# Kernel tuning notes

Measured on AMD Instinct MI355X. Metric: run time of the kernel, lower is better.

The kernel has to match this reference:

```python
import jax, jax.numpy as jnp
import numpy as np
from jax.ops import segment_sum

N = 100000   # nodes
E = 1600000  # edges
F = 128      # node feature dim
H = 128      # hidden dim
FE = 16      # edge feature dim
G = 256      # num graphs
EPS = 1e-5   # batch-norm eps


def setup_inputs() -> dict:
    key = jax.random.key(0)
    ks = jax.random.split(key, 16)
    s = 0.05
    return {
        "x": jax.random.normal(ks[0], (N, F), jnp.float32),
        "edge_index": jax.random.randint(ks[1], (2, E), 0, N, dtype=jnp.int32),
        "edge_attr": jax.random.normal(ks[2], (E, FE), jnp.float32),
        "batch_idx": jnp.sort(jax.random.randint(ks[3], (N,), 0, G, dtype=jnp.int32)),
        # GCN layer 1
        "W_g1": jax.random.normal(ks[4], (F, H), jnp.float32) * s,
        "b_g1": jnp.zeros((H,), jnp.float32),
        "gamma1": jnp.ones((H,), jnp.float32),
        "beta1": jnp.zeros((H,), jnp.float32),
        # GCN layer 2
        "W_g2": jax.random.normal(ks[5], (H, H), jnp.float32) * s,
        "b_g2": jnp.zeros((H,), jnp.float32),
        "gamma2": jnp.ones((H,), jnp.float32),
        "beta2": jnp.zeros((H,), jnp.float32),
        # edge encoder MLP
        "W_e1": jax.random.normal(ks[6], (FE, H), jnp.float32) * s,
        "b_e1": jnp.zeros((H,), jnp.float32),
        "W_e2": jax.random.normal(ks[7], (H, H), jnp.float32) * s,
        "b_e2": jnp.zeros((H,), jnp.float32),
    }


def _gcn_bn_relu(x, src, dst, W, b, gamma, beta):
    """GCNConv (sym-normalized, self-loops) + BatchNorm1d (batch stats) + ReLU."""
    h = x @ W                                             # [N, H]
    ones = jnp.ones((E,), h.dtype)
    deg = segment_sum(ones, dst, num_segments=N) + 1.0    # self-loop degree
    dinv = jax.lax.rsqrt(deg)                             # [N]
    norm = dinv[src] * dinv[dst]                          # [E]
    agg = segment_sum(h[src] * norm[:, None], dst, num_segments=N)
    out = agg + h * (dinv * dinv)[:, None] + b            # self-loop + bias
    mu = out.mean(axis=0)
    var = out.var(axis=0)
    out = (out - mu) * jax.lax.rsqrt(var + EPS) * gamma + beta
    return jax.nn.relu(out)


def reference(x, edge_index, edge_attr, batch_idx, W_g1, b_g1, gamma1, beta1,
              W_g2, b_g2, gamma2, beta2, W_e1, b_e1, W_e2, b_e2):
    src, dst = edge_index[0], edge_index[1]
    h = _gcn_bn_relu(x, src, dst, W_g1, b_g1, gamma1, beta1)
    h = _gcn_bn_relu(h, src, dst, W_g2, b_g2, gamma2, beta2)

    # global mean pool over nodes per graph
    node_cnt = segment_sum(jnp.ones((N,), h.dtype), batch_idx, num_segments=G)
    graph_repr = segment_sum(h, batch_idx, num_segments=G) / jnp.maximum(node_cnt, 1.0)[:, None]

    # edge encoder MLP + per-graph edge mean (vectorized version of the loop)
    e = jax.nn.relu(edge_attr @ W_e1 + b_e1) @ W_e2 + b_e2   # [E, H]
    edge_batch = batch_idx[src]                              # [E]
    edge_cnt = segment_sum(jnp.ones((E,), e.dtype), edge_batch, num_segments=G)
    edge_sum = segment_sum(e, edge_batch, num_segments=G)
    edge_repr = jnp.where(edge_cnt[:, None] > 0, edge_sum / jnp.maximum(edge_cnt, 1.0)[:, None], 0.0)

    return graph_repr + edge_repr  # [G, H]
```

## Files before the change

kernel.cpp:

```cpp
#include <hip/hip_runtime.h>
#include <cstdint>

__device__ inline unsigned int bfpack2(float a, float b) {
  unsigned int ua = __float_as_uint(a), ub = __float_as_uint(b);
  ua += 0x7FFFu + ((ua >> 16) & 1u);
  ub += 0x7FFFu + ((ub >> 16) & 1u);
  return (ua >> 16) | (ub & 0xFFFF0000u);
}
__device__ inline float bflo(unsigned int u) { return __uint_as_float(u << 16); }
__device__ inline float bfhi(unsigned int u) { return __uint_as_float(u & 0xFFFF0000u); }

__global__ __launch_bounds__(256) void pre_kernel(const int* __restrict__ src,
                                                  const int* __restrict__ dst,
                                                  int* __restrict__ deg,
                                                  int* __restrict__ deg2, int nE) {
  int e = blockIdx.x * 256 + threadIdx.x;
  if (e < nE) {
    atomicAdd(&deg[dst[e]], 1);
    atomicAdd(&deg2[src[e]], 1);
  }
}

__global__ __launch_bounds__(256) void scanA_kernel(const int* __restrict__ deg,
                                                    const int* __restrict__ deg2,
                                                    int* __restrict__ rp,
                                                    int* __restrict__ rp2,
                                                    int* __restrict__ part,
                                                    int* __restrict__ part2,
                                                    int n, int nb) {
  __shared__ int sh[256];
  int b = blockIdx.x, t = threadIdx.x;
  const int* d = (b < nb) ? deg : deg2;
  int* r = (b < nb) ? rp : rp2;
  int* p = (b < nb) ? part : part2;
  int pad = (b < nb) ? 1 : 0;
  int bb = (b < nb) ? b : b - nb;
  int base = bb * 1024 + t * 4;
  int v0 = (base + 0 < n) ? d[base + 0] : 0;
  int v1 = (base + 1 < n) ? d[base + 1] : 0;
  int v2 = (base + 2 < n) ? d[base + 2] : 0;
  int v3 = (base + 3 < n) ? d[base + 3] : 0;
  if (pad) {
    v0 = (v0 + 7) & ~7; v1 = (v1 + 7) & ~7;
    v2 = (v2 + 7) & ~7; v3 = (v3 + 7) & ~7;
  }
  int ts = v0 + v1 + v2 + v3;
  sh[t] = ts;
  __syncthreads();
  for (int off = 1; off < 256; off <<= 1) {
    int x = (t >= off) ? sh[t - off] : 0;
    __syncthreads();
    sh[t] += x;
    __syncthreads();
  }
  int excl = sh[t] - ts;
  if (t == 255) p[bb] = sh[255];
  if (base + 0 < n) r[base + 0] = excl;
  if (base + 1 < n) r[base + 1] = excl + v0;
  if (base + 2 < n) r[base + 2] = excl + v0 + v1;
  if (base + 3 < n) r[base + 3] = excl + v0 + v1 + v2;
}

__global__ void scanB_kernel(int* part, int* part2, int* rp, int* rp2, int nb, int n) {
  if (threadIdx.x == 0) {
    int* p = (blockIdx.x == 0) ? part : part2;
    int* r = (blockIdx.x == 0) ? rp : rp2;
    int run = 0;
    for (int i = 0; i < nb; ++i) { int v = p[i]; p[i] = run; run += v; }
    r[n] = run;
  }
}

__global__ __launch_bounds__(256) void scanC_kernel(int* __restrict__ rp,
                                                    int* __restrict__ rp2,
                                                    const int* __restrict__ part,
                                                    const int* __restrict__ part2,
                                                    int* __restrict__ cursor,
                                                    int* __restrict__ cursor2,
                                                    const int* __restrict__ deg,
                                                    float* __restrict__ dinv, int n) {
  int i = blockIdx.x * 256 + threadIdx.x;
  if (i < n) {
    int v = rp[i] + part[i >> 10];
    rp[i] = v;
    cursor[i] = v;
    dinv[i] = rsqrtf((float)deg[i] + 1.0f);
  } else if (i < 2 * n) {
    int j = i - n;
    int v = rp2[j] + part2[j >> 10];
    rp2[j] = v;
    cursor2[j] = v;
  }
}

__global__ __launch_bounds__(256) void placepad_kernel(const int* __restrict__ src,
                                                       const int* __restrict__ dst,
                                                       const int* __restrict__ batch,
                                                       const float* __restrict__ dinv,
                                                       int* __restrict__ cursor,
                                                       int* __restrict__ cursor2,
                                                       int2* __restrict__ swv,
                                                       unsigned int* __restrict__ epk,
                                                       const int* __restrict__ rp,
                                                       const int* __restrict__ deg,
                                                       int nE, int nN) {
  int t = blockIdx.x * 256 + threadIdx.x;
  if (t < nE) {
    int s = src[t];
    int d = dst[t];
    int p1 = atomicAdd(&cursor[d], 1);
    int2 sw; sw.x = s; sw.y = __float_as_int(dinv[s] * dinv[d]);
    swv[p1] = sw;
    int g = batch[s];
    int p2 = atomicAdd(&cursor2[s], 1);
    epk[p2] = ((unsigned int)g << 21) | (unsigned int)t;
  } else if (t < nE + nN) {
    int i = t - nE;
    int b = rp[i] + deg[i], e = rp[i + 1];
    int2 z; z.x = i; z.y = 0;
    for (int k = b; k < e; ++k) swv[k] = z;
  }
}

template <bool FUSED>
__global__ __launch_bounds__(256) void gemm128_kernel(const float* __restrict__ A,
                                                      const float* __restrict__ W,
                                                      const float* __restrict__ scale,
                                                      const float* __restrict__ shift,
                                                      unsigned int* __restrict__ hpk2,
                                                      int nrows) {
  extern __shared__ float lds[];
  float* Ws = lds;
  float* xs = lds + 128 * 128;
  const int t = threadIdx.x;
  for (int i = t; i < (128 * 128) / 4; i += 256)
    reinterpret_cast<float4*>(Ws)[i] = reinterpret_cast<const float4*>(W)[i];
  const int wave = t >> 6, lane = t & 63;
  const size_t sbase = (size_t)(lane >> 3) * (size_t)nrows * 8 + (lane & 7);
  for (int rb = blockIdx.x * 16; rb < nrows; rb += gridDim.x * 16) {
    int nr = min(16, nrows - rb);
    __syncthreads();
    for (int i = t; i < nr * 32; i += 256) {
      float4 v = reinterpret_cast<const float4*>(A + (size_t)rb * 128)[i];
      if (FUSED) {
        float4 sc4 = reinterpret_cast<const float4*>(scale)[i & 31];
        float4 sh4 = reinterpret_cast<const float4*>(shift)[i & 31];
        v.x = fmaxf(fmaf(v.x, sc4.x, sh4.x), 0.f);
        v.y = fmaxf(fmaf(v.y, sc4.y, sh4.y), 0.f);
        v.z = fmaxf(fmaf(v.z, sc4.z, sh4.z), 0.f);
        v.w = fmaxf(fmaf(v.w, sc4.w, sh4.w), 0.f);
      }
      reinterpret_cast<float4*>(xs)[i] = v;
    }
    __syncthreads();
    float acc[4][2] = {{0.f, 0.f}, {0.f, 0.f}, {0.f, 0.f}, {0.f, 0.f}};
    const float* xw = xs + wave * 4 * 128;
#pragma unroll 4
    for (int k = 0; k < 128; ++k) {
      float w0 = Ws[k * 128 + lane];
      float w1 = Ws[k * 128 + 64 + lane];
#pragma unroll
      for (int r = 0; r < 4; ++r) {
        float a = xw[r * 128 + k];
        acc[r][0] = fmaf(a, w0, acc[r][0]);
        acc[r][1] = fmaf(a, w1, acc[r][1]);
      }
    }
#pragma unroll
    for (int r = 0; r < 4; ++r) {
      int row = rb + wave * 4 + r;
      if (row < nrows)
        hpk2[sbase + (size_t)row * 8] = bfpack2(acc[r][0], acc[r][1]);
    }
  }
}

__global__ __launch_bounds__(256) void spmm8_kernel(const unsigned int* __restrict__ hpk2,
                                                    const float* __restrict__ dinv,
                                                    const int* __restrict__ rp,
                                                    const int2* __restrict__ swv,
                                                    const float* __restrict__ bias,
                                                    float* __restrict__ outp,
                                                    float* __restrict__ bnsum,
                                                    float* __restrict__ bnsq, int nN) {
  const int lane = threadIdx.x & 63;
  const int ch = lane & 7;
  const int es = lane >> 3;
  const int slice = blockIdx.x & 7;
  const unsigned int* hs = hpk2 + (size_t)slice * (size_t)nN * 8;
  const int cb = slice * 8;
  const int wib = (int)(blockIdx.x >> 3) * 4 + (int)(threadIdx.x >> 6);
  const int nws = (int)(gridDim.x >> 3) * 4;
  const unsigned long long* swq = reinterpret_cast<const unsigned long long*>(swv);
  float b0 = bias[cb + ch], b1 = bias[64 + cb + ch];
  float s0 = 0.f, s1 = 0.f, q0 = 0.f, q1 = 0.f;
  const int half = (nN + 1) >> 1;

#define SPMM_CHUNK(J, ACC0, ACC1)                                         \
  {                                                                       \
    unsigned long long v_ = __builtin_nontemporal_load(swq + (J) + es);   \
    unsigned int pp_ = hs[(size_t)(unsigned int)v_ * 8 + ch];             \
    float ww_ = __uint_as_float((unsigned int)(v_ >> 32));                \
    ACC0 = fmaf(ww_, bflo(pp_), ACC0);                                    \
    ACC1 = fmaf(ww_, bfhi(pp_), ACC1);                                    \
  }

  for (int p = wib; p < half; p += nws) {
    const int n0 = p;
    const int n1 = p + half;
    const bool has1 = n1 < nN;
    int j0 = rp[n0];
    const int end0 = rp[n0 + 1];
    int j1 = 0, end1 = 0;
    if (has1) { j1 = rp[n1]; end1 = rp[n1 + 1]; }
    float a00 = 0.f, a01 = 0.f, b00 = 0.f, b01 = 0.f;
    float a10 = 0.f, a11 = 0.f, b10 = 0.f, b11 = 0.f;
    while (j0 + 8 < end0 && j1 + 8 < end1) {
      SPMM_CHUNK(j0, a00, a01);
      SPMM_CHUNK(j0 + 8, b00, b01);
      SPMM_CHUNK(j1, a10, a11);
      SPMM_CHUNK(j1 + 8, b10, b11);
      j0 += 16; j1 += 16;
    }
    while (j0 + 8 < end0) {
      SPMM_CHUNK(j0, a00, a01);
      SPMM_CHUNK(j0 + 8, b00, b01);
      j0 += 16;
    }
    if (j0 < end0) SPMM_CHUNK(j0, a00, a01);
    while (j1 + 8 < end1) {
      SPMM_CHUNK(j1, a10, a11);
      SPMM_CHUNK(j1 + 8, b10, b11);
      j1 += 16;
    }
    if (j1 < end1) SPMM_CHUNK(j1, a10, a11);

    a00 += b00; a01 += b01;
    a10 += b10; a11 += b11;
    a00 += __shfl_xor(a00, 8);  a01 += __shfl_xor(a01, 8);
    a10 += __shfl_xor(a10, 8);  a11 += __shfl_xor(a11, 8);
    a00 += __shfl_xor(a00, 16); a01 += __shfl_xor(a01, 16);
    a10 += __shfl_xor(a10, 16); a11 += __shfl_xor(a11, 16);
    a00 += __shfl_xor(a00, 32); a01 += __shfl_xor(a01, 32);
    a10 += __shfl_xor(a10, 32); a11 += __shfl_xor(a11, 32);
    if (es == 0) {
      {
        float dn = dinv[n0];
        float sw = dn * dn;
        unsigned int pn = hs[(size_t)n0 * 8 + ch];
        float o0 = fmaf(bflo(pn), sw, a00) + b0;
        float o1 = fmaf(bfhi(pn), sw, a01) + b1;
        __builtin_nontemporal_store(o0, &outp[(size_t)n0 * 128 + cb + ch]);
        __builtin_nontemporal_store(o1, &outp[(size_t)n0 * 128 + 64 + cb + ch]);
        s0 += o0; s1 += o1;
        q0 = fmaf(o0, o0, q0); q1 = fmaf(o1, o1, q1);
      }
      if (has1) {
        float dn = dinv[n1];
        float sw = dn * dn;
        unsigned int pn = hs[(size_t)n1 * 8 + ch];
        float o0 = fmaf(bflo(pn), sw, a10) + b0;
        float o1 = fmaf(bfhi(pn), sw, a11) + b1;
        __builtin_nontemporal_store(o0, &outp[(size_t)n1 * 128 + cb + ch]);
        __builtin_nontemporal_store(o1, &outp[(size_t)n1 * 128 + 64 + cb + ch]);
        s0 += o0; s1 += o1;
        q0 = fmaf(o0, o0, q0); q1 = fmaf(o1, o1, q1);
      }
    }
  }
#undef SPMM_CHUNK
  if (es == 0) {
    atomicAdd(&bnsum[cb + ch], s0);
    atomicAdd(&bnsum[64 + cb + ch], s1);
    atomicAdd(&bnsq[cb + ch], q0);
    atomicAdd(&bnsq[64 + cb + ch], q1);
  }
}

__global__ void bnfin_kernel(const float* __restrict__ sum, const float* __restrict__ sq,
                             const float* __restrict__ gamma, const float* __restrict__ beta,
                             float* __restrict__ scale, float* __restrict__ shift,
                             float invN) {
  int c = threadIdx.x;
  float mu = sum[c] * invN;
  float var = sq[c] * invN - mu * mu;
  float sc = gamma[c] * rsqrtf(var + 1e-5f);
  scale[c] = sc;
  shift[c] = beta[c] - mu * sc;
}

__global__ __launch_bounds__(256) void pool_kernel(const float* __restrict__ h,
                                                   const int* __restrict__ batch,
                                                   const float* __restrict__ scale,
                                                   const float* __restrict__ shift,
                                                   float* __restrict__ gsum,
                                                   float* __restrict__ gcnt,
                                                   int nN, int chunk) {
  const int lane = threadIdx.x & 63;
  const int wid = (blockIdx.x * blockDim.x + threadIdx.x) >> 6;
  int beg = wid * chunk;
  if (beg >= nN) return;
  int end = min(nN, beg + chunk);
  const int c2 = 2 * lane;
  float2 sc2 = *reinterpret_cast<const float2*>(scale + c2);
  float2 sh2 = *reinterpret_cast<const float2*>(shift + c2);
  int cur = -1;
  float a0 = 0.f, a1 = 0.f, cnt = 0.f;
  for (int n = beg; n < end; ++n) {
    int g = batch[n];
    if (g != cur) {
      if (cur >= 0) {
        atomicAdd(&gsum[cur * 128 + c2], a0);
        atomicAdd(&gsum[cur * 128 + c2 + 1], a1);
        if (lane == 0) atomicAdd(&gcnt[cur], cnt);
      }
      cur = g; a0 = 0.f; a1 = 0.f; cnt = 0.f;
    }
    float2 v = *reinterpret_cast<const float2*>(h + (size_t)n * 128 + c2);
    a0 += fmaxf(fmaf(v.x, sc2.x, sh2.x), 0.f);
    a1 += fmaxf(fmaf(v.y, sc2.y, sh2.y), 0.f);
    cnt += 1.f;
  }
  if (cur >= 0) {
    atomicAdd(&gsum[cur * 128 + c2], a0);
    atomicAdd(&gsum[cur * 128 + c2 + 1], a1);
    if (lane == 0) atomicAdd(&gcnt[cur], cnt);
  }
}

#define MLP16(R0, R1, R2, R3, U0, U1)                          \
  do {                                                         \
    U0 = b0; U1 = b1;                                          \
    U0 = fmaf(R0.x, w0[0], U0);  U1 = fmaf(R0.x, w1[0], U1);   \
    U0 = fmaf(R0.y, w0[1], U0);  U1 = fmaf(R0.y, w1[1], U1);   \
    U0 = fmaf(R0.z, w0[2], U0);  U1 = fmaf(R0.z, w1[2], U1);   \
    U0 = fmaf(R0.w, w0[3], U0);  U1 = fmaf(R0.w, w1[3], U1);   \
    U0 = fmaf(R1.x, w0[4], U0);  U1 = fmaf(R1.x, w1[4], U1);   \
    U0 = fmaf(R1.y, w0[5], U0);  U1 = fmaf(R1.y, w1[5], U1);   \
    U0 = fmaf(R1.z, w0[6], U0);  U1 = fmaf(R1.z, w1[6], U1);   \
    U0 = fmaf(R1.w, w0[7], U0);  U1 = fmaf(R1.w, w1[7], U1);   \
    U0 = fmaf(R2.x, w0[8], U0);  U1 = fmaf(R2.x, w1[8], U1);   \
    U0 = fmaf(R2.y, w0[9], U0);  U1 = fmaf(R2.y, w1[9], U1);   \
    U0 = fmaf(R2.z, w0[10], U0); U1 = fmaf(R2.z, w1[10], U1);  \
    U0 = fmaf(R2.w, w0[11], U0); U1 = fmaf(R2.w, w1[11], U1);  \
    U0 = fmaf(R3.x, w0[12], U0); U1 = fmaf(R3.x, w1[12], U1);  \
    U0 = fmaf(R3.y, w0[13], U0); U1 = fmaf(R3.y, w1[13], U1);  \
    U0 = fmaf(R3.z, w0[14], U0); U1 = fmaf(R3.z, w1[14], U1);  \
    U0 = fmaf(R3.w, w0[15], U0); U1 = fmaf(R3.w, w1[15], U1);  \
  } while (0)

#define EFLUSH()                                               \
  do {                                                         \
    if (cur >= 0) {                                            \
      atomicAdd(&esum[cur * 128 + lane], a0);                  \
      atomicAdd(&esum[cur * 128 + 64 + lane], a1);             \
      if (lane == 0) atomicAdd(&ecnt[cur], cnt);               \
    }                                                          \
  } while (0)

#define ONE_EDGE(K)                                            \
  do {                                                         \
    int g_ = (int)((K) >> 21);                                 \
    if (g_ != cur) { EFLUSH(); cur = g_; a0 = 0.f; a1 = 0.f; cnt = 0.f; } \
    int e_ = (int)((K) & 0x1FFFFFu);                           \
    const float4* p_ = reinterpret_cast<const float4*>(ea + (size_t)e_ * 16); \
    float4 R0 = p_[0], R1 = p_[1], R2 = p_[2], R3 = p_[3];     \
    float u_, v_;                                              \
    MLP16(R0, R1, R2, R3, u_, v_);                             \
    a0 += fmaxf(u_, 0.f);                                      \
    a1 += fmaxf(v_, 0.f);                                      \
    cnt += 1.f;                                                \
  } while (0)

__global__ __launch_bounds__(256, 4) void edge4_kernel(const float* __restrict__ ea,
                                                       const unsigned int* __restrict__ epk,
                                                       const float* __restrict__ We1,
                                                       const float* __restrict__ be1,
                                                       float* __restrict__ esum,
                                                       float* __restrict__ ecnt,
                                                       int nE, int chunk) {
  const int lane = threadIdx.x & 63;
  const int wid = (blockIdx.x * 256 + threadIdx.x) >> 6;
  int beg = wid * chunk;
  if (beg >= nE) return;
  int end = min(nE, beg + chunk);
  float w0[16], w1[16];
#pragma unroll
  for (int k = 0; k < 16; ++k) {
    w0[k] = We1[k * 128 + lane];
    w1[k] = We1[k * 128 + 64 + lane];
  }
  float b0 = be1[lane], b1 = be1[64 + lane];
  int cur = -1;
  float a0 = 0.f, a1 = 0.f, cnt = 0.f;
  int j = beg;
  while (j + 4 <= end) {
    unsigned int k0 = epk[j], k1 = epk[j + 1], k2 = epk[j + 2], k3 = epk[j + 3];
    if ((((k0 ^ k1) | (k0 ^ k2) | (k0 ^ k3)) >> 21) == 0) {
      int g = (int)(k0 >> 21);
      if (g != cur) { EFLUSH(); cur = g; a0 = 0.f; a1 = 0.f; cnt = 0.f; }
      int e0 = (int)(k0 & 0x1FFFFFu), e1 = (int)(k1 & 0x1FFFFFu);
      int e2 = (int)(k2 & 0x1FFFFFu), e3 = (int)(k3 & 0x1FFFFFu);
      const float4* pA = reinterpret_cast<const float4*>(ea + (size_t)e0 * 16);
      const float4* pB = reinterpret_cast<const float4*>(ea + (size_t)e1 * 16);
      const float4* pC = reinterpret_cast<const float4*>(ea + (size_t)e2 * 16);
      const float4* pD = reinterpret_cast<const float4*>(ea + (size_t)e3 * 16);
      float4 A0 = pA[0], A1 = pA[1], A2 = pA[2], A3 = pA[3];
      float4 B0 = pB[0], B1 = pB[1], B2 = pB[2], B3 = pB[3];
      float4 C0 = pC[0], C1 = pC[1], C2 = pC[2], C3 = pC[3];
      float4 D0 = pD[0], D1 = pD[1], D2 = pD[2], D3 = pD[3];
      float uA0, uA1, uB0, uB1, uC0, uC1, uD0, uD1;
      MLP16(A0, A1, A2, A3, uA0, uA1);
      MLP16(B0, B1, B2, B3, uB0, uB1);
      MLP16(C0, C1, C2, C3, uC0, uC1);
      MLP16(D0, D1, D2, D3, uD0, uD1);
      a0 += fmaxf(uA0, 0.f) + fmaxf(uB0, 0.f) + fmaxf(uC0, 0.f) + fmaxf(uD0, 0.f);
      a1 += fmaxf(uA1, 0.f) + fmaxf(uB1, 0.f) + fmaxf(uC1, 0.f) + fmaxf(uD1, 0.f);
      cnt += 4.f;
      j += 4;
    } else {
      ONE_EDGE(k0);
      j += 1;
    }
  }
  while (j < end) {
    unsigned int k0 = epk[j];
    ONE_EDGE(k0);
    j += 1;
  }
  EFLUSH();
}

__global__ __launch_bounds__(128) void final_kernel(const float* __restrict__ gsum,
                                                    const float* __restrict__ gcnt,
                                                    const float* __restrict__ esum,
                                                    const float* __restrict__ ecnt,
                                                    const float* __restrict__ We2,
                                                    const float* __restrict__ be2,
                                                    float* __restrict__ out) {
  __shared__ float row[128];
  int g = blockIdx.x, c = threadIdx.x;
  row[c] = esum[g * 128 + c];
  __syncthreads();
  float acc = 0.f;
#pragma unroll 4
  for (int k = 0; k < 128; ++k) acc = fmaf(row[k], We2[k * 128 + c], acc);
  float ce = ecnt[g];
  float er = (ce > 0.f) ? (acc / ce + be2[c]) : 0.f;
  float cn = gcnt[g];
  float gr = gsum[g * 128 + c] / fmaxf(cn, 1.f);
  out[g * 128 + c] = gr + er;
}

extern "C" void kernel_launch(void* const* d_in, const int* in_sizes, int n_in,
                              void* d_out, int out_size, void* d_ws, size_t ws_size,
                              hipStream_t stream) {
  const float* x    = (const float*)d_in[0];
  const int*   ei   = (const int*)d_in[1];
  const float* ea   = (const float*)d_in[2];
  const int*   bidx = (const int*)d_in[3];
  const float* Wg1  = (const float*)d_in[4];
  const float* bg1  = (const float*)d_in[5];
  const float* gm1  = (const float*)d_in[6];
  const float* bt1  = (const float*)d_in[7];
  const float* Wg2  = (const float*)d_in[8];
  const float* bg2  = (const float*)d_in[9];
  const float* gm2  = (const float*)d_in[10];
  const float* bt2  = (const float*)d_in[11];
  const float* We1  = (const float*)d_in[12];
  const float* be1  = (const float*)d_in[13];
  const float* We2  = (const float*)d_in[14];
  const float* be2  = (const float*)d_in[15];
  float* out = (float*)d_out;

  const int N = in_sizes[3];
  const int E = in_sizes[1] / 2;
  const int G = out_size / 128;
  const int* srcp = ei;
  const int* dstp = ei + E;
  const int Epad = E + 8 * N;

  char* w = (char*)d_ws;
  auto alloc = [&](size_t b) {
    char* p = w;
    w += (b + 15) & ~(size_t)15;
    return p;
  };
  float* bufB    = (float*)alloc((size_t)N * 128 * 4);
  unsigned int* hpk2 = (unsigned int*)alloc((size_t)N * 64 * 4);
  int2*  swv     = (int2*)alloc((size_t)Epad * 8);
  unsigned int* epk = (unsigned int*)alloc((size_t)E * 4);
  int*   rp      = (int*)alloc((size_t)(N + 1) * 4);
  int*   rp2     = (int*)alloc((size_t)(N + 1) * 4);
  int*   cursor  = (int*)alloc((size_t)N * 4);
  int*   cursor2 = (int*)alloc((size_t)N * 4);
  float* dinv    = (float*)alloc((size_t)N * 4);
  char* zbase = w;
  int*   deg  = (int*)alloc((size_t)N * 4);
  int*   deg2 = (int*)alloc((size_t)N * 4);
  float* bs1  = (float*)alloc(512);
  float* bq1  = (float*)alloc(512);
  float* bs2  = (float*)alloc(512);
  float* bq2  = (float*)alloc(512);
  float* gsum = (float*)alloc((size_t)G * 128 * 4);
  float* gcnt = (float*)alloc((size_t)G * 4);
  float* esum = (float*)alloc((size_t)G * 128 * 4);
  float* ecnt = (float*)alloc((size_t)G * 4);
  int*   part  = (int*)alloc(4096);
  int*   part2 = (int*)alloc(4096);
  size_t zbytes = (size_t)(w - zbase);
  float* sc1 = (float*)alloc(512);
  float* sh1 = (float*)alloc(512);
  float* sc2 = (float*)alloc(512);
  float* sh2 = (float*)alloc(512);

  hipMemsetAsync(zbase, 0, zbytes, stream);

  (void)hipFuncSetAttribute((const void*)gemm128_kernel<false>,
                            hipFuncAttributeMaxDynamicSharedMemorySize, 73728);
  (void)hipFuncSetAttribute((const void*)gemm128_kernel<true>,
                            hipFuncAttributeMaxDynamicSharedMemorySize, 73728);

  pre_kernel<<<(E + 255) / 256, 256, 0, stream>>>(srcp, dstp, deg, deg2, E);
  int nb = (N + 1023) / 1024;
  scanA_kernel<<<2 * nb, 256, 0, stream>>>(deg, deg2, rp, rp2, part, part2, N, nb);
  scanB_kernel<<<2, 64, 0, stream>>>(part, part2, rp, rp2, nb, N);
  scanC_kernel<<<(2 * N + 255) / 256, 256, 0, stream>>>(rp, rp2, part, part2, cursor,
                                                        cursor2, deg, dinv, N);
  placepad_kernel<<<(E + N + 255) / 256, 256, 0, stream>>>(srcp, dstp, bidx, dinv, cursor,
                                                           cursor2, swv, epk, rp, deg, E, N);

  gemm128_kernel<false><<<512, 256, 73728, stream>>>(x, Wg1, nullptr, nullptr, hpk2, N);
  spmm8_kernel<<<2048, 256, 0, stream>>>(hpk2, dinv, rp, swv, bg1, bufB, bs1, bq1, N);
  bnfin_kernel<<<1, 128, 0, stream>>>(bs1, bq1, gm1, bt1, sc1, sh1, 1.0f / (float)N);

  gemm128_kernel<true><<<512, 256, 73728, stream>>>(bufB, Wg2, sc1, sh1, hpk2, N);
  spmm8_kernel<<<2048, 256, 0, stream>>>(hpk2, dinv, rp, swv, bg2, bufB, bs2, bq2, N);
  bnfin_kernel<<<1, 128, 0, stream>>>(bs2, bq2, gm2, bt2, sc2, sh2, 1.0f / (float)N);

  int nwp = (2048 * 256) / 64;
  int chunkN = (N + nwp - 1) / nwp;
  pool_kernel<<<2048, 256, 0, stream>>>(bufB, bidx, sc2, sh2, gsum, gcnt, N, chunkN);
  int nwe = (2048 * 256) / 64;
  int chunkE = (E + nwe - 1) / nwe;
  edge4_kernel<<<2048, 256, 0, stream>>>(ea, epk, We1, be1, esum, ecnt, E, chunkE);
  final_kernel<<<G, 128, 0, stream>>>(gsum, gcnt, esum, ecnt, We2, be2, out);
}
```

Measured before the change: 1.498 ms.

## Pre-scatter edge features into sorted order as bf16 for sequential edge MLP

```diff
diff --git a/kernel.cpp b/kernel.cpp
--- a/kernel.cpp
+++ b/kernel.cpp
@@ -101,6 +101,7 @@
                                                        int* __restrict__ cursor2,
                                                        int2* __restrict__ swv,
                                                        unsigned int* __restrict__ epk,
+                                                       int* __restrict__ pos2,
                                                        const int* __restrict__ rp,
                                                        const int* __restrict__ deg,
                                                        int nE, int nN) {
@@ -114,6 +115,7 @@
     int g = batch[s];
     int p2 = atomicAdd(&cursor2[s], 1);
     epk[p2] = ((unsigned int)g << 21) | (unsigned int)t;
+    pos2[t] = p2;
   } else if (t < nE + nN) {
     int i = t - nE;
     int b = rp[i] + deg[i], e = rp[i + 1];
@@ -328,57 +330,32 @@
   }
 }
 
-#define MLP16(R0, R1, R2, R3, U0, U1)                          \
-  do {                                                         \
-    U0 = b0; U1 = b1;                                          \
-    U0 = fmaf(R0.x, w0[0], U0);  U1 = fmaf(R0.x, w1[0], U1);   \
-    U0 = fmaf(R0.y, w0[1], U0);  U1 = fmaf(R0.y, w1[1], U1);   \
-    U0 = fmaf(R0.z, w0[2], U0);  U1 = fmaf(R0.z, w1[2], U1);   \
-    U0 = fmaf(R0.w, w0[3], U0);  U1 = fmaf(R0.w, w1[3], U1);   \
-    U0 = fmaf(R1.x, w0[4], U0);  U1 = fmaf(R1.x, w1[4], U1);   \
-    U0 = fmaf(R1.y, w0[5], U0);  U1 = fmaf(R1.y, w1[5], U1);   \
-    U0 = fmaf(R1.z, w0[6], U0);  U1 = fmaf(R1.z, w1[6], U1);   \
-    U0 = fmaf(R1.w, w0[7], U0);  U1 = fmaf(R1.w, w1[7], U1);   \
-    U0 = fmaf(R2.x, w0[8], U0);  U1 = fmaf(R2.x, w1[8], U1);   \
-    U0 = fmaf(R2.y, w0[9], U0);  U1 = fmaf(R2.y, w1[9], U1);   \
-    U0 = fmaf(R2.z, w0[10], U0); U1 = fmaf(R2.z, w1[10], U1);  \
-    U0 = fmaf(R2.w, w0[11], U0); U1 = fmaf(R2.w, w1[11], U1);  \
-    U0 = fmaf(R3.x, w0[12], U0); U1 = fmaf(R3.x, w1[12], U1);  \
-    U0 = fmaf(R3.y, w0[13], U0); U1 = fmaf(R3.y, w1[13], U1);  \
-    U0 = fmaf(R3.z, w0[14], U0); U1 = fmaf(R3.z, w1[14], U1);  \
-    U0 = fmaf(R3.w, w0[15], U0); U1 = fmaf(R3.w, w1[15], U1);  \
-  } while (0)
-
-#define EFLUSH()                                               \
-  do {                                                         \
-    if (cur >= 0) {                                            \
-      atomicAdd(&esum[cur * 128 + lane], a0);                  \
-      atomicAdd(&esum[cur * 128 + 64 + lane], a1);             \
-      if (lane == 0) atomicAdd(&ecnt[cur], cnt);               \
-    }                                                          \
-  } while (0)
-
-#define ONE_EDGE(K)                                            \
-  do {                                                         \
-    int g_ = (int)((K) >> 21);                                 \
-    if (g_ != cur) { EFLUSH(); cur = g_; a0 = 0.f; a1 = 0.f; cnt = 0.f; } \
-    int e_ = (int)((K) & 0x1FFFFFu);                           \
-    const float4* p_ = reinterpret_cast<const float4*>(ea + (size_t)e_ * 16); \
-    float4 R0 = p_[0], R1 = p_[1], R2 = p_[2], R3 = p_[3];     \
-    float u_, v_;                                              \
-    MLP16(R0, R1, R2, R3, u_, v_);                             \
-    a0 += fmaxf(u_, 0.f);                                      \
-    a1 += fmaxf(v_, 0.f);                                      \
-    cnt += 1.f;                                                \
-  } while (0)
-
-__global__ __launch_bounds__(256, 4) void edge4_kernel(const float* __restrict__ ea,
-                                                       const unsigned int* __restrict__ epk,
-                                                       const float* __restrict__ We1,
-                                                       const float* __restrict__ be1,
-                                                       float* __restrict__ esum,
-                                                       float* __restrict__ ecnt,
-                                                       int nE, int chunk) {
+__global__ __launch_bounds__(256) void scatter_kernel(const float* __restrict__ ea,
+                                                      const int* __restrict__ pos2,
+                                                      unsigned int* __restrict__ eah, int nE) {
+  int e = blockIdx.x * 256 + threadIdx.x;
+  if (e < nE) {
+    const float4* p = reinterpret_cast<const float4*>(ea + (size_t)e * 16);
+    float4 a = p[0], b = p[1], c = p[2], d = p[3];
+    uint4 o0, o1;
+    o0.x = bfpack2(a.x, a.y); o0.y = bfpack2(a.z, a.w);
+    o0.z = bfpack2(b.x, b.y); o0.w = bfpack2(b.z, b.w);
+    o1.x = bfpack2(c.x, c.y); o1.y = bfpack2(c.z, c.w);
+    o1.z = bfpack2(d.x, d.y); o1.w = bfpack2(d.z, d.w);
+    int j = pos2[e];
+    uint4* dst = reinterpret_cast<uint4*>(eah + (size_t)j * 8);
+    dst[0] = o0;
+    dst[1] = o1;
+  }
+}
+
+__global__ __launch_bounds__(256) void edge6_kernel(const unsigned int* __restrict__ eah,
+                                                    const unsigned int* __restrict__ epk,
+                                                    const float* __restrict__ We1,
+                                                    const float* __restrict__ be1,
+                                                    float* __restrict__ esum,
+                                                    float* __restrict__ ecnt,
+                                                    int nE, int chunk) {
   const int lane = threadIdx.x & 63;
   const int wid = (blockIdx.x * 256 + threadIdx.x) >> 6;
   int beg = wid * chunk;
@@ -393,42 +370,54 @@
   float b0 = be1[lane], b1 = be1[64 + lane];
   int cur = -1;
   float a0 = 0.f, a1 = 0.f, cnt = 0.f;
-  int j = beg;
-  while (j + 4 <= end) {
-    unsigned int k0 = epk[j], k1 = epk[j + 1], k2 = epk[j + 2], k3 = epk[j + 3];
-    if ((((k0 ^ k1) | (k0 ^ k2) | (k0 ^ k3)) >> 21) == 0) {
-      int g = (int)(k0 >> 21);
-      if (g != cur) { EFLUSH(); cur = g; a0 = 0.f; a1 = 0.f; cnt = 0.f; }
-      int e0 = (int)(k0 & 0x1FFFFFu), e1 = (int)(k1 & 0x1FFFFFu);
-      int e2 = (int)(k2 & 0x1FFFFFu), e3 = (int)(k3 & 0x1FFFFFu);
-      const float4* pA = reinterpret_cast<const float4*>(ea + (size_t)e0 * 16);
-      const float4* pB = reinterpret_cast<const float4*>(ea + (size_t)e1 * 16);
-      const float4* pC = reinterpret_cast<const float4*>(ea + (size_t)e2 * 16);
-      const float4* pD = reinterpret_cast<const float4*>(ea + (size_t)e3 * 16);
-      float4 A0 = pA[0], A1 = pA[1], A2 = pA[2], A3 = pA[3];
-      float4 B0 = pB[0], B1 = pB[1], B2 = pB[2], B3 = pB[3];
-      float4 C0 = pC[0], C1 = pC[1], C2 = pC[2], C3 = pC[3];
-      float4 D0 = pD[0], D1 = pD[1], D2 = pD[2], D3 = pD[3];
-      float uA0, uA1, uB0, uB1, uC0, uC1, uD0, uD1;
-      MLP16(A0, A1, A2, A3, uA0, uA1);
-      MLP16(B0, B1, B2, B3, uB0, uB1);
-      MLP16(C0, C1, C2, C3, uC0, uC1);
-      MLP16(D0, D1, D2, D3, uD0, uD1);
-      a0 += fmaxf(uA0, 0.f) + fmaxf(uB0, 0.f) + fmaxf(uC0, 0.f) + fmaxf(uD0, 0.f);
-      a1 += fmaxf(uA1, 0.f) + fmaxf(uB1, 0.f) + fmaxf(uC1, 0.f) + fmaxf(uD1, 0.f);
-      cnt += 4.f;
-      j += 4;
-    } else {
-      ONE_EDGE(k0);
-      j += 1;
-    }
-  }
-  while (j < end) {
-    unsigned int k0 = epk[j];
-    ONE_EDGE(k0);
-    j += 1;
-  }
-  EFLUSH();
+  const uint4* rowp = reinterpret_cast<const uint4*>(eah + (size_t)beg * 8);
+  uint4 q0 = rowp[0], q1 = rowp[1];
+  int g = (int)(epk[beg] >> 21);
+  for (int j = beg; j < end; ++j) {
+    uint4 n0, n1;
+    int ng = g;
+    if (j + 1 < end) {
+      const uint4* np = reinterpret_cast<const uint4*>(eah + (size_t)(j + 1) * 8);
+      n0 = np[0];
+      n1 = np[1];
+      ng = (int)(epk[j + 1] >> 21);
+    }
+    if (g != cur) {
+      if (cur >= 0) {
+        atomicAdd(&esum[cur * 128 + lane], a0);
+        atomicAdd(&esum[cur * 128 + 64 + lane], a1);
+        if (lane == 0) atomicAdd(&ecnt[cur], cnt);
+      }
+      cur = g; a0 = 0.f; a1 = 0.f; cnt = 0.f;
+    }
+    float u0 = b0, u1 = b1;
+    float f;
+    f = bflo(q0.x); u0 = fmaf(f, w0[0], u0);  u1 = fmaf(f, w1[0], u1);
+    f = bfhi(q0.x); u0 = fmaf(f, w0[1], u0);  u1 = fmaf(f, w1[1], u1);
+    f = bflo(q0.y); u0 = fmaf(f, w0[2], u0);  u1 = fmaf(f, w1[2], u1);
+    f = bfhi(q0.y); u0 = fmaf(f, w0[3], u0);  u1 = fmaf(f, w1[3], u1);
+    f = bflo(q0.z); u0 = fmaf(f, w0[4], u0);  u1 = fmaf(f, w1[4], u1);
+    f = bfhi(q0.z); u0 = fmaf(f, w0[5], u0);  u1 = fmaf(f, w1[5], u1);
+    f = bflo(q0.w); u0 = fmaf(f, w0[6], u0);  u1 = fmaf(f, w1[6], u1);
+    f = bfhi(q0.w); u0 = fmaf(f, w0[7], u0);  u1 = fmaf(f, w1[7], u1);
+    f = bflo(q1.x); u0 = fmaf(f, w0[8], u0);  u1 = fmaf(f, w1[8], u1);
+    f = bfhi(q1.x); u0 = fmaf(f, w0[9], u0);  u1 = fmaf(f, w1[9], u1);
+    f = bflo(q1.y); u0 = fmaf(f, w0[10], u0); u1 = fmaf(f, w1[10], u1);
+    f = bfhi(q1.y); u0 = fmaf(f, w0[11], u0); u1 = fmaf(f, w1[11], u1);
+    f = bflo(q1.z); u0 = fmaf(f, w0[12], u0); u1 = fmaf(f, w1[12], u1);
+    f = bfhi(q1.z); u0 = fmaf(f, w0[13], u0); u1 = fmaf(f, w1[13], u1);
+    f = bflo(q1.w); u0 = fmaf(f, w0[14], u0); u1 = fmaf(f, w1[14], u1);
+    f = bfhi(q1.w); u0 = fmaf(f, w0[15], u0); u1 = fmaf(f, w1[15], u1);
+    a0 += fmaxf(u0, 0.f);
+    a1 += fmaxf(u1, 0.f);
+    cnt += 1.f;
+    q0 = n0; q1 = n1; g = ng;
+  }
+  if (cur >= 0) {
+    atomicAdd(&esum[cur * 128 + lane], a0);
+    atomicAdd(&esum[cur * 128 + 64 + lane], a1);
+    if (lane == 0) atomicAdd(&ecnt[cur], cnt);
+  }
 }
 
 __global__ __launch_bounds__(128) void final_kernel(const float* __restrict__ gsum,
@@ -490,6 +479,7 @@
   unsigned int* hpk2 = (unsigned int*)alloc((size_t)N * 64 * 4);
   int2*  swv     = (int2*)alloc((size_t)Epad * 8);
   unsigned int* epk = (unsigned int*)alloc((size_t)E * 4);
+  int*   pos2    = (int*)alloc((size_t)E * 4);
   int*   rp      = (int*)alloc((size_t)(N + 1) * 4);
   int*   rp2     = (int*)alloc((size_t)(N + 1) * 4);
   int*   cursor  = (int*)alloc((size_t)N * 4);
@@ -514,6 +504,8 @@
   float* sc2 = (float*)alloc(512);
   float* sh2 = (float*)alloc(512);
 
+  unsigned int* eah = (unsigned int*)bufB;
+
   hipMemsetAsync(zbase, 0, zbytes, stream);
 
   (void)hipFuncSetAttribute((const void*)gemm128_kernel<false>,
@@ -528,7 +520,8 @@
   scanC_kernel<<<(2 * N + 255) / 256, 256, 0, stream>>>(rp, rp2, part, part2, cursor,
                                                         cursor2, deg, dinv, N);
   placepad_kernel<<<(E + N + 255) / 256, 256, 0, stream>>>(srcp, dstp, bidx, dinv, cursor,
-                                                           cursor2, swv, epk, rp, deg, E, N);
+                                                           cursor2, swv, epk, pos2, rp, deg,
+                                                           E, N);
 
   gemm128_kernel<false><<<512, 256, 73728, stream>>>(x, Wg1, nullptr, nullptr, hpk2, N);
   spmm8_kernel<<<2048, 256, 0, stream>>>(hpk2, dinv, rp, swv, bg1, bufB, bs1, bq1, N);
@@ -541,8 +534,11 @@
   int nwp = (2048 * 256) / 64;
   int chunkN = (N + nwp - 1) / nwp;
   pool_kernel<<<2048, 256, 0, stream>>>(bufB, bidx, sc2, sh2, gsum, gcnt, N, chunkN);
+
+  scatter_kernel<<<(E + 255) / 256, 256, 0, stream>>>(ea, pos2, eah, E);
   int nwe = (2048 * 256) / 64;
   int chunkE = (E + nwe - 1) / nwe;
-  edge4_kernel<<<2048, 256, 0, stream>>>(ea, epk, We1, be1, esum, ecnt, E, chunkE);
+  edge6_kernel<<<2048, 256, 0, stream>>>(eah, epk, We1, be1, esum, ecnt, E, chunkE);
+
   final_kernel<<<G, 128, 0, stream>>>(gsum, gcnt, esum, ecnt, We2, be2, out);
 }
```

New measurement: 1.236 ms. 1.21x faster.
